# Kernel optimization log

Hardware: AMD Instinct MI355X
Metric: run time of the kernel (lower is better)

The kernel has to match this reference:

```python
import jax, jax.numpy as jnp
import numpy as np

B, S, D = 16, 2048, 128

def setup_inputs() -> dict:
    key = jax.random.key(0)
    kq, kk, kv = jax.random.split(key, 3)
    queries = jax.random.normal(kq, (B, S, D), dtype=jnp.float32)
    keys = jax.random.normal(kk, (B, S, D), dtype=jnp.float32)
    values = jax.random.normal(kv, (B, S, D), dtype=jnp.float32)
    return {"queries": queries, "keys": keys, "values": values}

def reference(queries, keys, values):
    # scores: [B, S, S] = Q @ K^T / sqrt(D)
    d = queries.shape[-1]
    scores = jnp.einsum('bqd,bkd->bqk', queries, keys) / jnp.float32(np.sqrt(d))
    attn = jax.nn.softmax(scores, axis=-1)
    # dropout_rate=0.0 -> identity
    out = jnp.einsum('bqk,bkd->bqd', attn, values)
    return out
```

## Files before the change

### kernel.cpp

```cpp
#include <hip/hip_runtime.h>
#include <hip/hip_bf16.h>

#define BATCH 16
#define SEQ   2048
#define DIM   128
#define KTILE 64
#define NIT   (SEQ / KTILE)
#define QT    128
#define SCALE 0.08838834764831845f

typedef __bf16 bf16_t;
typedef __bf16 bf16x8 __attribute__((ext_vector_type(8)));
typedef __bf16 bf16x4 __attribute__((ext_vector_type(4)));
typedef float  f32x4  __attribute__((ext_vector_type(4)));

#define KSTR 136

__device__ __forceinline__ int rho(int s) {
    return (s & 32) | ((s & 4) << 2) | (((s >> 3) & 3) << 2) | (s & 3);
}
__device__ __forceinline__ int swz(int row) {
    return (row & 7) ^ ((row >> 2) & 7);
}

__global__ __launch_bounds__(512, 2)
void attn_fwd(const float* __restrict__ Qg, const float* __restrict__ Kg,
              const float* __restrict__ Vg, float* __restrict__ Og)
{
    __shared__ __align__(16) bf16_t sK [2][KTILE][KSTR];
    __shared__ __align__(16) bf16_t sVt[2][DIM][64];

    const int tid  = threadIdx.x;
    const int wave = tid >> 6;
    const int lane = tid & 63;
    const int l16  = lane & 15;
    const int g    = lane >> 4;

    const int bid   = blockIdx.x;
    const int batch = ((bid & 7) << 1) | ((bid >> 7) & 1);
    const int qtile = (bid >> 3) & 15;
    const int q0    = qtile * QT + wave * 16;

    const float* Kb = Kg + (size_t)batch * SEQ * DIM;
    const float* Vb = Vg + (size_t)batch * SEQ * DIM;

    bf16x8 qf[4];
    {
        const float* qp = Qg + ((size_t)batch * SEQ + q0 + l16) * DIM + g * 8;
        #pragma unroll
        for (int c = 0; c < 4; ++c) {
            const float4 u = *reinterpret_cast<const float4*>(qp + c * 32);
            const float4 v = *reinterpret_cast<const float4*>(qp + c * 32 + 4);
            bf16x8 f;
            f[0] = (bf16_t)(u.x * SCALE); f[1] = (bf16_t)(u.y * SCALE);
            f[2] = (bf16_t)(u.z * SCALE); f[3] = (bf16_t)(u.w * SCALE);
            f[4] = (bf16_t)(v.x * SCALE); f[5] = (bf16_t)(v.y * SCALE);
            f[6] = (bf16_t)(v.z * SCALE); f[7] = (bf16_t)(v.w * SCALE);
            qf[c] = f;
        }
    }

    const int krow = tid >> 3;
    const int kch  = tid & 7;
    const int vkg  = tid >> 5;
    const int vd4  = tid & 31;

    float4 ka[2][2];
    float4 va[4];

    auto load_tile = [&](int k0) {
        #pragma unroll
        for (int i = 0; i < 2; ++i) {
            const float* p = Kb + (size_t)(k0 + krow) * DIM + kch * 8 + i * 64;
            ka[i][0] = *reinterpret_cast<const float4*>(p);
            ka[i][1] = *reinterpret_cast<const float4*>(p + 4);
        }
        #pragma unroll
        for (int j = 0; j < 4; ++j)
            va[j] = *reinterpret_cast<const float4*>(
                Vb + (size_t)(k0 + vkg * 4 + j) * DIM + vd4 * 4);
    };
    auto write_tile = [&](int buf) {
        #pragma unroll
        for (int i = 0; i < 2; ++i) {
            const float* a = reinterpret_cast<const float*>(&ka[i][0]);
            bf16x8 w;
            #pragma unroll
            for (int e = 0; e < 8; ++e) w[e] = (bf16_t)a[e];
            *reinterpret_cast<bf16x8*>(&sK[buf][rho(krow)][kch * 8 + i * 64]) = w;
        }
        #pragma unroll
        for (int dd = 0; dd < 4; ++dd) {
            const int row = vd4 * 4 + dd;
            const int col = (((vkg >> 1) ^ swz(row)) << 3) + ((vkg & 1) << 2);
            bf16x4 w;
            w[0] = (bf16_t)va[0][dd]; w[1] = (bf16_t)va[1][dd];
            w[2] = (bf16_t)va[2][dd]; w[3] = (bf16_t)va[3][dd];
            *reinterpret_cast<bf16x4*>(&sVt[buf][row][col]) = w;
        }
    };

    const f32x4 vzero = {0.f, 0.f, 0.f, 0.f};
    f32x4 o[8];
    #pragma unroll
    for (int i = 0; i < 8; ++i) o[i] = vzero;
    float lsum = 0.f;

    load_tile(0);
    write_tile(0);
    load_tile(KTILE);

    for (int it = 0; it < NIT; ++it) {
        __syncthreads();

        if (it + 1 < NIT) {
            write_tile((it + 1) & 1);
            if (it + 2 < NIT) load_tile((it + 2) * KTILE);
        }
        const int cur = it & 1;

        f32x4 sc[4];
        #pragma unroll
        for (int ksb = 0; ksb < 4; ++ksb) sc[ksb] = vzero;
        #pragma unroll
        for (int c = 0; c < 4; ++c) {
            #pragma unroll
            for (int ksb = 0; ksb < 4; ++ksb) {
                bf16x8 kf = *reinterpret_cast<const bf16x8*>(
                    &sK[cur][ksb * 16 + l16][c * 32 + g * 8]);
                sc[ksb] = __builtin_amdgcn_mfma_f32_16x16x32_bf16(
                    kf, qf[c], sc[ksb], 0, 0, 0);
            }
        }

        float pe[16];
        #pragma unroll
        for (int ksb = 0; ksb < 4; ++ksb) {
            #pragma unroll
            for (int r = 0; r < 4; ++r) {
                const float p = __expf(sc[ksb][r]);
                pe[ksb * 4 + r] = p;
                lsum += p;
            }
        }
        bf16x8 pb[2];
        #pragma unroll
        for (int c2 = 0; c2 < 2; ++c2) {
            bf16x8 t;
            #pragma unroll
            for (int jj = 0; jj < 8; ++jj)
                t[jj] = (bf16_t)pe[(2 * c2 + (jj >> 2)) * 4 + (jj & 3)];
            pb[c2] = t;
        }

        #pragma unroll
        for (int n0 = 0; n0 < 8; ++n0) {
            const int row = n0 * 16 + l16;
            #pragma unroll
            for (int c2 = 0; c2 < 2; ++c2) {
                bf16x8 vf = *reinterpret_cast<const bf16x8*>(
                    &sVt[cur][row][((c2 * 4 + g) ^ swz(row)) << 3]);
                o[n0] = __builtin_amdgcn_mfma_f32_16x16x32_bf16(
                    vf, pb[c2], o[n0], 0, 0, 0);
            }
        }
    }

    float l = lsum;
    l += __shfl_xor(l, 16);
    l += __shfl_xor(l, 32);
    const float inv = 1.f / l;
    float* op = Og + ((size_t)batch * SEQ + q0 + l16) * DIM + g * 4;
    #pragma unroll
    for (int n0 = 0; n0 < 8; ++n0) {
        float4 st = { o[n0][0] * inv, o[n0][1] * inv,
                      o[n0][2] * inv, o[n0][3] * inv };
        *reinterpret_cast<float4*>(op + n0 * 16) = st;
    }
}

extern "C" void kernel_launch(void* const* d_in, const int* in_sizes, int n_in,
                              void* d_out, int out_size, void* d_ws, size_t ws_size,
                              hipStream_t stream) {
    const float* Q = (const float*)d_in[0];
    const float* K = (const float*)d_in[1];
    const float* V = (const float*)d_in[2];
    float* O = (float*)d_out;
    dim3 grid(BATCH * SEQ / QT);
    dim3 block(512);
    hipLaunchKernelGGL(attn_fwd, grid, block, 0, stream, Q, K, V, O);
}
```

Before: 134.4 us.

## Split key range across two blocks and combine partial attention outputs

Splits each query tile's key sequence into two halves processed by separate blocks, doubling the grid from 256 to 512 blocks so all CUs can be occupied. Each half writes unnormalized partial outputs and row sums to workspace, and a second combine kernel adds them and normalizes. It also changes the V-transpose swizzle, writes V to shared memory as scalar stores, and raises launch bounds to 4 blocks per CU. The cost is extra global traffic (two full-size fp32 partial outputs written and reread) plus a second launch. Softmax has no max subtraction, so partials combine by simple addition.

```diff
diff --git a/kernel.cpp b/kernel.cpp
--- a/kernel.cpp
+++ b/kernel.cpp
@@ -5,27 +5,30 @@
 #define SEQ   2048
 #define DIM   128
 #define KTILE 64
-#define NIT   (SEQ / KTILE)
-#define QT    128
 #define SCALE 0.08838834764831845f
 
 typedef __bf16 bf16_t;
 typedef __bf16 bf16x8 __attribute__((ext_vector_type(8)));
-typedef __bf16 bf16x4 __attribute__((ext_vector_type(4)));
 typedef float  f32x4  __attribute__((ext_vector_type(4)));
 
 #define KSTR 136
+
+#define HALF_O  (BATCH * SEQ * DIM)
+#define HALF_L  (BATCH * SEQ)
+#define WS_NEED ((size_t)(2 * HALF_O + 2 * HALF_L) * 4)
 
 __device__ __forceinline__ int rho(int s) {
     return (s & 32) | ((s & 4) << 2) | (((s >> 3) & 3) << 2) | (s & 3);
 }
-__device__ __forceinline__ int swz(int row) {
-    return (row & 7) ^ ((row >> 2) & 7);
-}
-
-__global__ __launch_bounds__(512, 2)
+__device__ __forceinline__ int swz2(int row) {
+    return (row & 7) ^ ((row >> 3) & 7);
+}
+
+template <int SPLIT>
+__global__ __launch_bounds__(512, 4)
 void attn_fwd(const float* __restrict__ Qg, const float* __restrict__ Kg,
-              const float* __restrict__ Vg, float* __restrict__ Og)
+              const float* __restrict__ Vg, float* __restrict__ Op,
+              float* __restrict__ lp)
 {
     __shared__ __align__(16) bf16_t sK [2][KTILE][KSTR];
     __shared__ __align__(16) bf16_t sVt[2][DIM][64];
@@ -37,9 +40,13 @@
     const int g    = lane >> 4;
 
     const int bid   = blockIdx.x;
-    const int batch = ((bid & 7) << 1) | ((bid >> 7) & 1);
-    const int qtile = (bid >> 3) & 15;
-    const int q0    = qtile * QT + wave * 16;
+    const int batch = SPLIT ? (((bid & 7) << 1) | ((bid >> 8) & 1))
+                            : (((bid & 7) << 1) | ((bid >> 7) & 1));
+    const int gr    = SPLIT ? ((bid >> 3) & 1) : 0;
+    const int qtile = SPLIT ? ((bid >> 4) & 15) : ((bid >> 3) & 15);
+    const int q0    = qtile * 128 + wave * 16;
+    const int kbeg  = gr * (SEQ / 2);
+    const int nit   = SPLIT ? (SEQ / 2 / KTILE) : (SEQ / KTILE);
 
     const float* Kb = Kg + (size_t)batch * SEQ * DIM;
     const float* Vb = Vg + (size_t)batch * SEQ * DIM;
@@ -92,11 +99,11 @@
         #pragma unroll
         for (int dd = 0; dd < 4; ++dd) {
             const int row = vd4 * 4 + dd;
-            const int col = (((vkg >> 1) ^ swz(row)) << 3) + ((vkg & 1) << 2);
-            bf16x4 w;
-            w[0] = (bf16_t)va[0][dd]; w[1] = (bf16_t)va[1][dd];
-            w[2] = (bf16_t)va[2][dd]; w[3] = (bf16_t)va[3][dd];
-            *reinterpret_cast<bf16x4*>(&sVt[buf][row][col]) = w;
+            const int col = (((vkg >> 1) ^ swz2(row)) << 3) + ((vkg & 1) << 2);
+            bf16_t w0 = (bf16_t)va[0][dd], w1 = (bf16_t)va[1][dd];
+            bf16_t w2 = (bf16_t)va[2][dd], w3 = (bf16_t)va[3][dd];
+            bf16_t* p = &sVt[buf][row][col];
+            p[0] = w0; p[1] = w1; p[2] = w2; p[3] = w3;
         }
     };
 
@@ -106,16 +113,15 @@
     for (int i = 0; i < 8; ++i) o[i] = vzero;
     float lsum = 0.f;
 
-    load_tile(0);
+    load_tile(kbeg);
     write_tile(0);
-    load_tile(KTILE);
-
-    for (int it = 0; it < NIT; ++it) {
+    load_tile(kbeg + KTILE);
+
+    for (int it = 0; it < nit; ++it) {
         __syncthreads();
-
-        if (it + 1 < NIT) {
+        if (it + 1 < nit) {
             write_tile((it + 1) & 1);
-            if (it + 2 < NIT) load_tile((it + 2) * KTILE);
+            if (it + 2 < nit) load_tile(kbeg + (it + 2) * KTILE);
         }
         const int cur = it & 1;
 
@@ -135,14 +141,13 @@
 
         float pe[16];
         #pragma unroll
-        for (int ksb = 0; ksb < 4; ++ksb) {
+        for (int ksb = 0; ksb < 4; ++ksb)
             #pragma unroll
             for (int r = 0; r < 4; ++r) {
                 const float p = __expf(sc[ksb][r]);
                 pe[ksb * 4 + r] = p;
                 lsum += p;
             }
-        }
         bf16x8 pb[2];
         #pragma unroll
         for (int c2 = 0; c2 < 2; ++c2) {
@@ -159,7 +164,7 @@
             #pragma unroll
             for (int c2 = 0; c2 < 2; ++c2) {
                 bf16x8 vf = *reinterpret_cast<const bf16x8*>(
-                    &sVt[cur][row][((c2 * 4 + g) ^ swz(row)) << 3]);
+                    &sVt[cur][row][((c2 * 4 + g) ^ swz2(row)) << 3]);
                 o[n0] = __builtin_amdgcn_mfma_f32_16x16x32_bf16(
                     vf, pb[c2], o[n0], 0, 0, 0);
             }
@@ -169,13 +174,45 @@
     float l = lsum;
     l += __shfl_xor(l, 16);
     l += __shfl_xor(l, 32);
-    const float inv = 1.f / l;
-    float* op = Og + ((size_t)batch * SEQ + q0 + l16) * DIM + g * 4;
+    const size_t rowbase = (size_t)batch * SEQ + q0 + l16;
+    if (SPLIT) {
+        float* op = Op + (size_t)gr * HALF_O + rowbase * DIM + g * 4;
+        #pragma unroll
+        for (int n0 = 0; n0 < 8; ++n0) {
+            float4 st = { o[n0][0], o[n0][1], o[n0][2], o[n0][3] };
+            *reinterpret_cast<float4*>(op + n0 * 16) = st;
+        }
+        if (g == 0) lp[gr * HALF_L + rowbase] = l;
+    } else {
+        const float inv = 1.f / l;
+        float* op = Op + rowbase * DIM + g * 4;
+        #pragma unroll
+        for (int n0 = 0; n0 < 8; ++n0) {
+            float4 st = { o[n0][0] * inv, o[n0][1] * inv,
+                          o[n0][2] * inv, o[n0][3] * inv };
+            *reinterpret_cast<float4*>(op + n0 * 16) = st;
+        }
+    }
+}
+
+__global__ __launch_bounds__(256)
+void attn_combine(const float* __restrict__ Op, const float* __restrict__ lp,
+                  float* __restrict__ out)
+{
+    const float4* A = reinterpret_cast<const float4*>(Op);
+    const float4* B = reinterpret_cast<const float4*>(Op + HALF_O);
+    float4* O4 = reinterpret_cast<float4*>(out);
+    const int t = blockIdx.x * 256 + threadIdx.x;
     #pragma unroll
-    for (int n0 = 0; n0 < 8; ++n0) {
-        float4 st = { o[n0][0] * inv, o[n0][1] * inv,
-                      o[n0][2] * inv, o[n0][3] * inv };
-        *reinterpret_cast<float4*>(op + n0 * 16) = st;
+    for (int j = 0; j < 8; ++j) {
+        const int idx = t + j * 131072;
+        const int row = idx >> 5;
+        const float inv = 1.f / (lp[row] + lp[HALF_L + row]);
+        const float4 a = A[idx];
+        const float4 b = B[idx];
+        float4 r = { (a.x + b.x) * inv, (a.y + b.y) * inv,
+                     (a.z + b.z) * inv, (a.w + b.w) * inv };
+        O4[idx] = r;
     }
 }
 
@@ -186,7 +223,15 @@
     const float* K = (const float*)d_in[1];
     const float* V = (const float*)d_in[2];
     float* O = (float*)d_out;
-    dim3 grid(BATCH * SEQ / QT);
-    dim3 block(512);
-    hipLaunchKernelGGL(attn_fwd, grid, block, 0, stream, Q, K, V, O);
-}
+    if (ws_size >= WS_NEED) {
+        float* Op = (float*)d_ws;
+        float* lp = Op + 2 * HALF_O;
+        hipLaunchKernelGGL(attn_fwd<1>, dim3(512), dim3(512), 0, stream,
+                           Q, K, V, Op, lp);
+        hipLaunchKernelGGL(attn_combine, dim3(512), dim3(256), 0, stream,
+                           Op, lp, O);
+    } else {
+        hipLaunchKernelGGL(attn_fwd<0>, dim3(256), dim3(512), 0, stream,
+                           Q, K, V, O, (float*)nullptr);
+    }
+}
```

Result: slower. 144.5 us (+7.5%).
